# Optimization experiments

Measured on AMD Instinct MI355X. Metric: run time of the kernel, lower is better.

## Reference

```python
import jax, jax.numpy as jnp
import numpy as np

B, S, D, H, DFF = 2, 2048, 1024, 16, 4096
DK = D // H
EPS = 1e-5


def layer_norm(x, gamma, beta, eps=EPS):
    mu = jnp.mean(x, axis=-1, keepdims=True)
    var = jnp.mean(jnp.square(x - mu), axis=-1, keepdims=True)
    return (x - mu) * jax.lax.rsqrt(var + eps) * gamma + beta


def setup_inputs() -> dict:
    key = jax.random.key(0)
    ks = jax.random.split(key, 12)
    s_d = 1.0 / np.sqrt(D)
    s_f = 1.0 / np.sqrt(DFF)
    return {
        "x": jax.random.normal(ks[0], (B, S, D), jnp.float32),
        # per-head QKV projections stacked: [H, D, DK]
        "Wq": jax.random.normal(ks[1], (H, D, DK), jnp.float32) * s_d,
        "bq": jnp.zeros((H, DK), jnp.float32),
        "Wk": jax.random.normal(ks[2], (H, D, DK), jnp.float32) * s_d,
        "bk": jnp.zeros((H, DK), jnp.float32),
        "Wv": jax.random.normal(ks[3], (H, D, DK), jnp.float32) * s_d,
        "bv": jnp.zeros((H, DK), jnp.float32),
        "Wo": jax.random.normal(ks[4], (D, D), jnp.float32) * s_d,
        "bo": jnp.zeros((D,), jnp.float32),
        "W1": jax.random.normal(ks[5], (D, DFF), jnp.float32) * s_d,
        "b1": jnp.zeros((DFF,), jnp.float32),
        "W2": jax.random.normal(ks[6], (DFF, D), jnp.float32) * s_f,
        "b2": jnp.zeros((D,), jnp.float32),
        "ln1_g": jnp.ones((D,), jnp.float32),
        "ln1_b": jnp.zeros((D,), jnp.float32),
        "ln2_g": jnp.ones((D,), jnp.float32),
        "ln2_b": jnp.zeros((D,), jnp.float32),
    }


def reference(x, Wq, bq, Wk, bk, Wv, bv, Wo, bo, W1, b1, W2, b2,
              ln1_g, ln1_b, ln2_g, ln2_b):
    # --- residual 1: pre-norm multi-head self-attention (mask unused, dropout=eval) ---
    h = layer_norm(x, ln1_g, ln1_b)                      # [B,S,D]
    q = jnp.einsum('bsd,hdk->bhsk', h, Wq) + bq[:, None, :]
    k = jnp.einsum('bsd,hdk->bhsk', h, Wk) + bk[:, None, :]
    v = jnp.einsum('bsd,hdk->bhsk', h, Wv) + bv[:, None, :]
    scores = jnp.einsum('bhsk,bhtk->bhst', q, k) / np.sqrt(DK)  # [B,H,S,S]
    w = jax.nn.softmax(scores, axis=-1)
    ctx = jnp.einsum('bhst,bhtk->bhsk', w, v)            # [B,H,S,DK]
    # concat heads along feature dim -> [B,S,D]
    ctx = jnp.transpose(ctx, (0, 2, 1, 3)).reshape(B, S, D)
    attn_out = ctx @ Wo + bo
    x = x + attn_out
    # --- residual 2: pre-norm feed-forward ---
    h2 = layer_norm(x, ln2_g, ln2_b)
    ff = jax.nn.relu(h2 @ W1 + b1) @ W2 + b2
    return x + ff
```

## Files before the change

kernel.cpp:

```cpp
#include <hip/hip_runtime.h>

#define B_   2
#define S_   2048
#define D_   1024
#define H_   16
#define DK_  64
#define DFF_ 4096
#define NT_  (B_*S_)
#define QS_  3072

using u16 = unsigned short;
typedef __attribute__((ext_vector_type(8))) short bf16x8;
typedef __attribute__((ext_vector_type(4))) float f32x4;
typedef __attribute__((ext_vector_type(4))) u16  u16x4;

__device__ __forceinline__ float bf2f(u16 h) {
  union { unsigned u; float f; } c; c.u = ((unsigned)h) << 16; return c.f;
}
__device__ __forceinline__ u16 f2bf(float f) {
  union { float f; unsigned u; } c; c.f = f;
  unsigned u = c.u;
  return (u16)((u + 0x7fffu + ((u >> 16) & 1u)) >> 16);
}
__device__ __forceinline__ u16 f2bf_up(float f) {
  union { float f; unsigned u; } c; c.f = f;
  return (u16)((c.u + 0x8000u) >> 16);
}

__device__ __forceinline__ void load_lds16(const void* g, void* l) {
  __builtin_amdgcn_global_load_lds(
      (const __attribute__((address_space(1))) unsigned int*)g,
      (__attribute__((address_space(3))) unsigned int*)l, 16, 0, 0);
}

__device__ __forceinline__ void store_out(u16* p, float v)   { *p = f2bf(v); }
__device__ __forceinline__ void store_out(float* p, float v) { *p = v; }

__global__ __launch_bounds__(256) void ln_kernel(
    const float* __restrict__ x, const float* __restrict__ g,
    const float* __restrict__ bt, u16* __restrict__ o)
{
  const int row = blockIdx.x, t = threadIdx.x;
  const float4 xv = *(const float4*)(x + (size_t)row * D_ + t * 4);
  float f[4] = {xv.x, xv.y, xv.z, xv.w};
  float sum = f[0] + f[1] + f[2] + f[3];
  float sq  = f[0]*f[0] + f[1]*f[1] + f[2]*f[2] + f[3]*f[3];
#pragma unroll
  for (int d = 32; d >= 1; d >>= 1) {
    sum += __shfl_down(sum, d);
    sq  += __shfl_down(sq, d);
  }
  __shared__ float red[8];
  const int lane = t & 63, wid = t >> 6;
  if (lane == 0) { red[wid] = sum; red[wid + 4] = sq; }
  __syncthreads();
  sum = red[0] + red[1] + red[2] + red[3];
  sq  = red[4] + red[5] + red[6] + red[7];
  const float mu   = sum * (1.0f / D_);
  const float var  = sq * (1.0f / D_) - mu * mu;
  const float rstd = rsqrtf(var + 1e-5f);
  const float4 gv = *(const float4*)(g  + t * 4);
  const float4 bv = *(const float4*)(bt + t * 4);
  u16x4 ov;
  ov[0] = f2bf((f[0] - mu) * rstd * gv.x + bv.x);
  ov[1] = f2bf((f[1] - mu) * rstd * gv.y + bv.y);
  ov[2] = f2bf((f[2] - mu) * rstd * gv.z + bv.z);
  ov[3] = f2bf((f[3] - mu) * rstd * gv.w + bv.w);
  *(u16x4*)(o + (size_t)row * D_ + t * 4) = ov;
}

__global__ __launch_bounds__(256) void transpose_h(
    const float* __restrict__ in, u16* __restrict__ out, int R, int C)
{
  __shared__ float tile[32][33];
  const int z = blockIdx.z;
  const float* ip = in  + (size_t)z * R * C;
  u16*         op = out + (size_t)z * R * C;
  const int c0 = blockIdx.x * 32, r0 = blockIdx.y * 32;
  const int tx = threadIdx.x & 31, ty = threadIdx.x >> 5;
#pragma unroll
  for (int i = 0; i < 32; i += 8)
    tile[ty + i][tx] = ip[(size_t)(r0 + ty + i) * C + c0 + tx];
  __syncthreads();
#pragma unroll
  for (int i = 0; i < 32; i += 8)
    op[(size_t)(c0 + ty + i) * R + r0 + tx] = f2bf(tile[tx][ty + i]);
}

__global__ __launch_bounds__(256) void transpose_qkv(
    const float* __restrict__ Wq, const float* __restrict__ Wk,
    const float* __restrict__ Wv, u16* __restrict__ out)
{
  __shared__ float tile[32][33];
  const int z = blockIdx.z;
  const int which = z >> 4, h = z & 15;
  const float* ip = (which == 0 ? Wq : which == 1 ? Wk : Wv) + (size_t)h * 1024 * 64;
  u16* op = out + ((size_t)which * 1024 + h * 64) * 1024;
  const float sc = (which == 0) ? 0.125f : 1.0f;
  const int c0 = blockIdx.x * 32, r0 = blockIdx.y * 32;
  const int tx = threadIdx.x & 31, ty = threadIdx.x >> 5;
#pragma unroll
  for (int i = 0; i < 32; i += 8)
    tile[ty + i][tx] = ip[(size_t)(r0 + ty + i) * 64 + c0 + tx];
  __syncthreads();
#pragma unroll
  for (int i = 0; i < 32; i += 8)
    op[(size_t)(c0 + ty + i) * 1024 + r0 + tx] = f2bf(tile[tx][ty + i] * sc);
}

__global__ __launch_bounds__(256) void pack_kv(
    const u16* __restrict__ qkv, u16* __restrict__ kt, u16* __restrict__ vt)
{
  __shared__ u16 tile[32][72];
  const int z = blockIdx.y;
  const int b = z >> 4, h = z & 15;
  const int t0 = blockIdx.x * 32;
  const int tid = threadIdx.x;
  const int row = tid >> 3, sub = tid & 7;

  const u16* src = qkv + (size_t)(b * S_ + t0 + row) * QS_ + h * DK_ + sub * 8;
  *(bf16x8*)(kt + ((size_t)z * S_ + t0 + row) * 64 + sub * 8) =
      *(const bf16x8*)(src + 1024);
  *(bf16x8*)&tile[row][sub * 8] = *(const bf16x8*)(src + 2048);
  __syncthreads();

  const int d = tid >> 2, tc = (tid & 3) * 8;
  bf16x8 val;
#pragma unroll
  for (int j = 0; j < 8; ++j) val[j] = (short)tile[tc + j][d];
  *(bf16x8*)(vt + ((size_t)z * 64 + d) * S_ + t0 + tc) = val;
}

template <typename OT, int KK>
__global__ __launch_bounds__(512, 1) void gemm256(
    const u16* __restrict__ A, const u16* __restrict__ Bt,
    const float* __restrict__ bias, const float* __restrict__ biasB,
    const float* __restrict__ biasC, OT* __restrict__ C,
    int M, int N, int do_relu)
{
  constexpr int NK = KK / 32;
  __shared__ u16 lA[4][256 * 32];
  __shared__ u16 lB[4][256 * 32];
  const int tid = threadIdx.x, lane = tid & 63, wid = tid >> 6;
  const int wr = wid >> 2, wc = wid & 3;

  const int nbx = gridDim.x;
  int bid = blockIdx.y * nbx + blockIdx.x;
  const int cpx = (nbx * gridDim.y) >> 3;
  bid = (bid & 7) * cpx + (bid >> 3);
  const int row0 = (bid / nbx) * 256, col0 = (bid % nbx) * 256;

  const int c0 = tid,       sr0 = c0 >> 2, q0 = ((c0 & 3) ^ (((sr0 >> 3) & 1) << 1)) * 8;
  const int c1 = tid + 512, sr1 = c1 >> 2, q1 = ((c1 & 3) ^ (((sr1 >> 3) & 1) << 1)) * 8;
  const u16* As0 = A  + (size_t)(row0 + sr0) * KK + q0;
  const u16* As1 = A  + (size_t)(row0 + sr1) * KK + q1;
  const u16* Bs0 = Bt + (size_t)(col0 + sr0) * KK + q0;
  const u16* Bs1 = Bt + (size_t)(col0 + sr1) * KK + q1;

  f32x4 acc[8][4] = {};
  const int lrow = lane & 15, kcol = (lane >> 4) * 8;

#pragma unroll
  for (int t = 0; t < 3; ++t) {
    load_lds16(As0 + t * 32, &lA[t][c0 * 8]);
    load_lds16(Bs0 + t * 32, &lB[t][c0 * 8]);
    load_lds16(As1 + t * 32, &lA[t][c1 * 8]);
    load_lds16(Bs1 + t * 32, &lB[t][c1 * 8]);
  }
  asm volatile("s_waitcnt vmcnt(8)" ::: "memory");
  __builtin_amdgcn_sched_barrier(0);
  __builtin_amdgcn_s_barrier();

#pragma unroll 4
  for (int j = 0; j < NK; ++j) {
    const int b = j & 3;
    const u16* la = lA[b];
    const u16* lb = lB[b];
    bf16x8 af[4], bfr[4];

#pragma unroll
    for (int m = 0; m < 4; ++m) {
      const int row = wr * 128 + m * 16 + lrow;
      af[m] = *(const bf16x8*)&la[row * 32 + (kcol ^ (((row >> 3) & 1) << 4))];
    }
#pragma unroll
    for (int n = 0; n < 4; ++n) {
      const int row = wc * 64 + n * 16 + lrow;
      bfr[n] = *(const bf16x8*)&lb[row * 32 + (kcol ^ (((row >> 3) & 1) << 4))];
    }
    if (j + 3 < NK) {
      const int bb = (j + 3) & 3;
      load_lds16(As0 + (j + 3) * 32, &lA[bb][c0 * 8]);
      load_lds16(Bs0 + (j + 3) * 32, &lB[bb][c0 * 8]);
    }
    __builtin_amdgcn_s_setprio(1);
#pragma unroll
    for (int m = 0; m < 4; ++m)
#pragma unroll
      for (int n = 0; n < 4; ++n)
        acc[m][n] = __builtin_amdgcn_mfma_f32_16x16x32_bf16(af[m], bfr[n], acc[m][n], 0, 0, 0);
    __builtin_amdgcn_s_setprio(0);

#pragma unroll
    for (int m = 0; m < 4; ++m) {
      const int row = wr * 128 + (m + 4) * 16 + lrow;
      af[m] = *(const bf16x8*)&la[row * 32 + (kcol ^ (((row >> 3) & 1) << 4))];
    }
    if (j + 3 < NK) {
      const int bb = (j + 3) & 3;
      load_lds16(As1 + (j + 3) * 32, &lA[bb][c1 * 8]);
      load_lds16(Bs1 + (j + 3) * 32, &lB[bb][c1 * 8]);
    }
    __builtin_amdgcn_s_setprio(1);
#pragma unroll
    for (int m = 0; m < 4; ++m)
#pragma unroll
      for (int n = 0; n < 4; ++n)
        acc[m + 4][n] = __builtin_amdgcn_mfma_f32_16x16x32_bf16(af[m], bfr[n], acc[m + 4][n], 0, 0, 0);
    __builtin_amdgcn_s_setprio(0);
    if (j + 3 < NK)      { asm volatile("s_waitcnt vmcnt(8)" ::: "memory"); }
    else if (j + 2 < NK) { asm volatile("s_waitcnt vmcnt(4)" ::: "memory"); }
    else if (j + 1 < NK) { asm volatile("s_waitcnt vmcnt(0)" ::: "memory"); }
    __builtin_amdgcn_sched_barrier(0);
    __builtin_amdgcn_s_barrier();
  }

#pragma unroll
  for (int m = 0; m < 8; ++m)
#pragma unroll
    for (int n = 0; n < 4; ++n) {
      const int rbase = row0 + wr*128 + m*16 + ((lane >> 4) << 2);
      const int c     = col0 + wc*64 + n*16 + (lane & 15);
      float bv = 0.f;
      if (biasC)      bv = c < 1024 ? bias[c] * 0.125f
                         : (c < 2048 ? biasB[c - 1024] : biasC[c - 2048]);
      else if (bias)  bv = bias[c];
#pragma unroll
      for (int r = 0; r < 4; ++r) {
        float vv = acc[m][n][r] + bv;
        if (do_relu) vv = vv > 0.f ? vv : 0.f;
        store_out(&C[(size_t)(rbase + r) * N + c], vv);
      }
    }
}

template <int KK>
__global__ __launch_bounds__(512, 1) void gemm256pk(
    const u16* __restrict__ A, const u16* __restrict__ Bt,
    u16* __restrict__ P, int M, int N, int Ktot)
{
  constexpr int NK = KK / 32;
  __shared__ u16 lA[4][256 * 32];
  __shared__ u16 lB[4][256 * 32];
  const int tid = threadIdx.x, lane = tid & 63, wid = tid >> 6;
  const int wr = wid >> 2, wc = wid & 3;

  const int nbx = gridDim.x;
  int bid = blockIdx.y * nbx + blockIdx.x;
  const int cpx = (nbx * gridDim.y) >> 3;
  bid = (bid & 7) * cpx + (bid >> 3);
  const int row0 = (bid / nbx) * 256, col0 = (bid % nbx) * 256;
  const int kb = blockIdx.z * KK;

  const int c0 = tid,       sr0 = c0 >> 2, q0 = ((c0 & 3) ^ (((sr0 >> 3) & 1) << 1)) * 8;
  const int c1 = tid + 512, sr1 = c1 >> 2, q1 = ((c1 & 3) ^ (((sr1 >> 3) & 1) << 1)) * 8;
  const u16* As0 = A  + (size_t)(row0 + sr0) * Ktot + kb + q0;
  const u16* As1 = A  + (size_t)(row0 + sr1) * Ktot + kb + q1;
  const u16* Bs0 = Bt + (size_t)(col0 + sr0) * Ktot + kb + q0;
  const u16* Bs1 = Bt + (size_t)(col0 + sr1) * Ktot + kb + q1;

  f32x4 acc[8][4] = {};
  const int lrow = lane & 15, kcol = (lane >> 4) * 8;

#pragma unroll
  for (int t = 0; t < 3; ++t) {
    load_lds16(As0 + t * 32, &lA[t][c0 * 8]);
    load_lds16(Bs0 + t * 32, &lB[t][c0 * 8]);
    load_lds16(As1 + t * 32, &lA[t][c1 * 8]);
    load_lds16(Bs1 + t * 32, &lB[t][c1 * 8]);
  }
  asm volatile("s_waitcnt vmcnt(8)" ::: "memory");
  __builtin_amdgcn_sched_barrier(0);
  __builtin_amdgcn_s_barrier();

#pragma unroll 4
  for (int j = 0; j < NK; ++j) {
    const int b = j & 3;
    const u16* la = lA[b];
    const u16* lb = lB[b];
    bf16x8 af[4], bfr[4];

#pragma unroll
    for (int m = 0; m < 4; ++m) {
      const int row = wr * 128 + m * 16 + lrow;
      af[m] = *(const bf16x8*)&la[row * 32 + (kcol ^ (((row >> 3) & 1) << 4))];
    }
#pragma unroll
    for (int n = 0; n < 4; ++n) {
      const int row = wc * 64 + n * 16 + lrow;
      bfr[n] = *(const bf16x8*)&lb[row * 32 + (kcol ^ (((row >> 3) & 1) << 4))];
    }
    if (j + 3 < NK) {
      const int bb = (j + 3) & 3;
      load_lds16(As0 + (j + 3) * 32, &lA[bb][c0 * 8]);
      load_lds16(Bs0 + (j + 3) * 32, &lB[bb][c0 * 8]);
    }
    __builtin_amdgcn_s_setprio(1);
#pragma unroll
    for (int m = 0; m < 4; ++m)
#pragma unroll
      for (int n = 0; n < 4; ++n)
        acc[m][n] = __builtin_amdgcn_mfma_f32_16x16x32_bf16(af[m], bfr[n], acc[m][n], 0, 0, 0);
    __builtin_amdgcn_s_setprio(0);

#pragma unroll
    for (int m = 0; m < 4; ++m) {
      const int row = wr * 128 + (m + 4) * 16 + lrow;
      af[m] = *(const bf16x8*)&la[row * 32 + (kcol ^ (((row >> 3) & 1) << 4))];
    }
    if (j + 3 < NK) {
      const int bb = (j + 3) & 3;
      load_lds16(As1 + (j + 3) * 32, &lA[bb][c1 * 8]);
      load_lds16(Bs1 + (j + 3) * 32, &lB[bb][c1 * 8]);
    }
    __builtin_amdgcn_s_setprio(1);
#pragma unroll
    for (int m = 0; m < 4; ++m)
#pragma unroll
      for (int n = 0; n < 4; ++n)
        acc[m + 4][n] = __builtin_amdgcn_mfma_f32_16x16x32_bf16(af[m], bfr[n], acc[m + 4][n], 0, 0, 0);
    __builtin_amdgcn_s_setprio(0);
    if (j + 3 < NK)      { asm volatile("s_waitcnt vmcnt(8)" ::: "memory"); }
    else if (j + 2 < NK) { asm volatile("s_waitcnt vmcnt(4)" ::: "memory"); }
    else if (j + 1 < NK) { asm volatile("s_waitcnt vmcnt(0)" ::: "memory"); }
    __builtin_amdgcn_sched_barrier(0);
    __builtin_amdgcn_s_barrier();
  }

  u16* Pz = P + (size_t)blockIdx.z * M * N;
#pragma unroll
  for (int m = 0; m < 8; ++m)
#pragma unroll
    for (int n = 0; n < 4; ++n) {
      const int rbase = row0 + wr*128 + m*16 + ((lane >> 4) << 2);
      const int c     = col0 + wc*64 + n*16 + (lane & 15);
#pragma unroll
      for (int r = 0; r < 4; ++r)
        Pz[(size_t)(rbase + r) * N + c] = f2bf(acc[m][n][r]);
    }
}

template <typename OT>
__global__ __launch_bounds__(256) void gemm_bt64(
    const u16* __restrict__ A, const u16* __restrict__ Bt,
    const float* __restrict__ bias, const float* __restrict__ res,
    OT* __restrict__ C, int M, int N, int K, int do_relu)
{
  __shared__ u16 lA[2][128 * 32];
  __shared__ u16 lB[2][64 * 32];
  const int tid = threadIdx.x, lane = tid & 63, wid = tid >> 6;

  const int nbx = gridDim.x;
  int bid = blockIdx.y * nbx + blockIdx.x;
  const int cpx = (nbx * gridDim.y) >> 3;
  bid = (bid & 7) * cpx + (bid >> 3);
  const int row0 = (bid / nbx) * 128, col0 = (bid % nbx) * 64;

  f32x4 acc[2][4] = {};

  const int cc0 = tid, cc1 = tid + 256;
  const int r0 = cc0 >> 2, s0 = cc0 & 3;
  const int r1 = cc1 >> 2, s1 = cc1 & 3;
  const int ko0 = (s0 ^ ((r0 >> 1) & 3)) * 8;
  const int ko1 = (s1 ^ ((r1 >> 1) & 3)) * 8;

#define GST64(bf, k0)                                                         \
  {                                                                           \
    load_lds16(A  + (size_t)(row0 + r0) * K + (k0) + ko0, &lA[bf][cc0 * 8]);  \
    load_lds16(A  + (size_t)(row0 + r1) * K + (k0) + ko1, &lA[bf][cc1 * 8]);  \
    load_lds16(Bt + (size_t)(col0 + r0) * K + (k0) + ko0, &lB[bf][cc0 * 8]);  \
  }

  const int nk = K >> 5;
  GST64(0, 0);
  int cur = 0;
  for (int t = 0; t < nk; ++t) {
    __syncthreads();
    if (t + 1 < nk) GST64(cur ^ 1, (t + 1) * 32);
    bf16x8 af[2], bfr[4];
#pragma unroll
    for (int m = 0; m < 2; ++m) {
      const int row = wid * 32 + m * 16 + (lane & 15);
      af[m] = *(const bf16x8*)&lA[cur][row * 32 + (((lane >> 4) ^ ((row >> 1) & 3)) * 8)];
    }
#pragma unroll
    for (int n = 0; n < 4; ++n) {
      const int row = n * 16 + (lane & 15);
      bfr[n] = *(const bf16x8*)&lB[cur][row * 32 + (((lane >> 4) ^ ((row >> 1) & 3)) * 8)];
    }
#pragma unroll
    for (int m = 0; m < 2; ++m)
#pragma unroll
      for (int n = 0; n < 4; ++n)
        acc[m][n] = __builtin_amdgcn_mfma_f32_16x16x32_bf16(af[m], bfr[n], acc[m][n], 0, 0, 0);
    cur ^= 1;
  }
#undef GST64

#pragma unroll
  for (int m = 0; m < 2; ++m)
#pragma unroll
    for (int n = 0; n < 4; ++n) {
      const int rbase = row0 + wid*32 + m*16 + ((lane >> 4) << 2);
      const int c     = col0 + n*16 + (lane & 15);
      const float bv  = bias ? bias[c] : 0.f;
#pragma unroll
      for (int r = 0; r < 4; ++r) {
        const int rr = rbase + r;
        float vv = acc[m][n][r] + bv;
        if (res) vv += res[(size_t)rr * N + c];
        if (do_relu) vv = vv > 0.f ? vv : 0.f;
        store_out(&C[(size_t)rr * N + c], vv);
      }
    }
}

__global__ __launch_bounds__(256) void ffr_reduce4(
    const u16* __restrict__ P, const float* __restrict__ x1,
    const float* __restrict__ b2, float* __restrict__ out)
{
  const size_t i = (size_t)blockIdx.x * 256 + threadIdx.x;
  const size_t M4 = (size_t)NT_ * D_;
  const float4 r  = ((const float4*)x1)[i];
  const float4 bb = ((const float4*)b2)[i & 255];
  float o0 = r.x + bb.x, o1 = r.y + bb.y, o2 = r.z + bb.z, o3 = r.w + bb.w;
#pragma unroll
  for (int z = 0; z < 4; ++z) {
    const u16x4 p = *(const u16x4*)(P + z * M4 + i * 4);
    o0 += bf2f(p[0]); o1 += bf2f(p[1]); o2 += bf2f(p[2]); o3 += bf2f(p[3]);
  }
  float4 o; o.x = o0; o.y = o1; o.z = o2; o.w = o3;
  ((float4*)out)[i] = o;
}

__global__ __launch_bounds__(512) void attn_kernel(
    const u16* __restrict__ QKV, const u16* __restrict__ Kt,
    const u16* __restrict__ Vt, u16* __restrict__ O)
{
  __shared__ u16 lK[2][64 * 64];
  __shared__ u16 lV[2][64 * 64];
  __shared__ u16 lP[128 * 64];

  const int tid = threadIdx.x, lane = tid & 63, wid = tid >> 6;
  const int g  = (blockIdx.x & 7) * 64 + (blockIdx.x >> 3);
  const int qt = g & 15, h = (g >> 4) & 15, b = g >> 8;
  const int z  = b * H_ + h;

  const u16* Qp  = QKV + (size_t)(b * S_ + qt * 128) * QS_ + h * DK_;
  const u16* Kpb = Kt + (size_t)z * S_ * 64;
  const u16* Vb  = Vt + (size_t)z * DK_ * S_;

  bf16x8 qf[2];
  {
    const int qr = wid * 16 + (lane & 15);
    qf[0] = *(const bf16x8*)(Qp + (size_t)qr * QS_ + (lane >> 4) * 8);
    qf[1] = *(const bf16x8*)(Qp + (size_t)qr * QS_ + 32 + (lane >> 4) * 8);
  }

  const bf16x8 vone = {16256,16256,16256,16256,16256,16256,16256,16256};

#define STAGE_KV(bf, kt_)                                                     \
  {                                                                           \
    const u16* Kp = Kpb + (size_t)(kt_) * 64 * 64;                            \
    const u16* Vp = Vb + (size_t)(kt_) * 64;                                  \
    const int c = tid, r = c >> 3, sub = c & 7;                               \
    load_lds16(Kp + r * 64 + ((sub ^ (r & 7)) * 8), &lK[bf][c * 8]);          \
    load_lds16(Vp + (size_t)r * S_ + ((sub ^ (r & 7)) * 8), &lV[bf][c * 8]);  \
  }

  float m_run = -1e30f;
  f32x4 l_acc = {};
  f32x4 o_acc[4] = {};

  STAGE_KV(0, 0);
  int cur = 0;

  for (int kt = 0; kt < S_ / 64; ++kt) {
    __syncthreads();
    if (kt + 1 < S_ / 64) STAGE_KV(cur ^ 1, kt + 1);

    f32x4 s[4];
    __builtin_amdgcn_s_setprio(1);
#pragma unroll
    for (int kf = 0; kf < 4; ++kf) {
      const int row = kf * 16 + (lane & 15);
      const int i0 = (row * 64 + (lane >> 4) * 8)      ^ ((row & 7) << 3);
      const int i1 = (row * 64 + 32 + (lane >> 4) * 8) ^ ((row & 7) << 3);
      bf16x8 k0 = *(const bf16x8*)&lK[cur][i0];
      bf16x8 k1 = *(const bf16x8*)&lK[cur][i1];
      f32x4 sc = {};
      sc = __builtin_amdgcn_mfma_f32_16x16x32_bf16(k0, qf[0], sc, 0, 0, 0);
      sc = __builtin_amdgcn_mfma_f32_16x16x32_bf16(k1, qf[1], sc, 0, 0, 0);
      s[kf] = sc;
    }
    __builtin_amdgcn_s_setprio(0);

    float t0 = fmaxf(fmaxf(s[0][0], s[0][1]), fmaxf(s[0][2], s[0][3]));
    float t1 = fmaxf(fmaxf(s[1][0], s[1][1]), fmaxf(s[1][2], s[1][3]));
    float t2 = fmaxf(fmaxf(s[2][0], s[2][1]), fmaxf(s[2][2], s[2][3]));
    float t3 = fmaxf(fmaxf(s[3][0], s[3][1]), fmaxf(s[3][2], s[3][3]));
    float pmax = fmaxf(fmaxf(t0, t1), fmaxf(t2, t3));
    pmax = fmaxf(pmax, __shfl_xor(pmax, 16));
    pmax = fmaxf(pmax, __shfl_xor(pmax, 32));

    const bool grow = pmax > m_run + 8.0f;
    const float mnew = grow ? pmax : m_run;
    if (__any(grow)) {
      const float scale = __expf(m_run - mnew);
#pragma unroll
      for (int r = 0; r < 4; ++r) {
        const float sr = __shfl(scale, (lane >> 4) * 4 + r);
        l_acc[r] *= sr;
#pragma unroll
        for (int nf = 0; nf < 4; ++nf) o_acc[nf][r] *= sr;
      }
    }
    m_run = mnew;

    const int prow = wid * 16 + (lane & 15);
#pragma unroll
    for (int kf = 0; kf < 4; ++kf) {
      u16x4 pk;
#pragma unroll
      for (int r = 0; r < 4; ++r) pk[r] = f2bf_up(__expf(s[kf][r] - m_run));
      const int idx = (prow * 64 + kf * 16 + (lane >> 4) * 4) ^ ((prow & 7) << 3);
      *(u16x4*)&lP[idx] = pk;
    }
    asm volatile("s_waitcnt lgkmcnt(0)" ::: "memory");
    __builtin_amdgcn_sched_barrier(0);

    bf16x8 pa0 = *(const bf16x8*)&lP[(prow * 64 + (lane >> 4) * 8)      ^ ((prow & 7) << 3)];
    bf16x8 pa1 = *(const bf16x8*)&lP[(prow * 64 + 32 + (lane >> 4) * 8) ^ ((prow & 7) << 3)];
    __builtin_amdgcn_s_setprio(1);
    l_acc = __builtin_amdgcn_mfma_f32_16x16x32_bf16(pa0, vone, l_acc, 0, 0, 0);
    l_acc = __builtin_amdgcn_mfma_f32_16x16x32_bf16(pa1, vone, l_acc, 0, 0, 0);
#pragma unroll
    for (int nf = 0; nf < 4; ++nf) {
      const int vrow = nf * 16 + (lane & 15);
      bf16x8 v0 = *(const bf16x8*)&lV[cur][(vrow * 64 + (lane >> 4) * 8)      ^ ((vrow & 7) << 3)];
      bf16x8 v1 = *(const bf16x8*)&lV[cur][(vrow * 64 + 32 + (lane >> 4) * 8) ^ ((vrow & 7) << 3)];
      o_acc[nf] = __builtin_amdgcn_mfma_f32_16x16x32_bf16(pa0, v0, o_acc[nf], 0, 0, 0);
      o_acc[nf] = __builtin_amdgcn_mfma_f32_16x16x32_bf16(pa1, v1, o_acc[nf], 0, 0, 0);
    }
    __builtin_amdgcn_s_setprio(0);
    cur ^= 1;
  }

#pragma unroll
  for (int nf = 0; nf < 4; ++nf)
#pragma unroll
    for (int r = 0; r < 4; ++r) {
      const int qrow = qt * 128 + wid * 16 + (lane >> 4) * 4 + r;
      const int col  = h * DK_ + nf * 16 + (lane & 15);
      O[(size_t)(b * S_ + qrow) * D_ + col] = f2bf(o_acc[nf][r] / l_acc[r]);
    }
}

extern "C" void kernel_launch(void* const* d_in, const int* in_sizes, int n_in,
                              void* d_out, int out_size, void* d_ws, size_t ws_size,
                              hipStream_t stream)
{
  const float* x   = (const float*)d_in[0];
  const float* Wq  = (const float*)d_in[1];
  const float* bq  = (const float*)d_in[2];
  const float* Wk  = (const float*)d_in[3];
  const float* bk  = (const float*)d_in[4];
  const float* Wv  = (const float*)d_in[5];
  const float* bv  = (const float*)d_in[6];
  const float* Wo  = (const float*)d_in[7];
  const float* bo  = (const float*)d_in[8];
  const float* W1  = (const float*)d_in[9];
  const float* b1  = (const float*)d_in[10];
  const float* W2  = (const float*)d_in[11];
  const float* b2  = (const float*)d_in[12];
  const float* g1  = (const float*)d_in[13];
  const float* be1 = (const float*)d_in[14];
  const float* g2  = (const float*)d_in[15];
  const float* be2 = (const float*)d_in[16];
  float* out = (float*)d_out;

  const size_t MB = 1024 * 1024;
  char* base = (char*)d_ws;
  u16*   xn    = (u16*)(base);
  u16*   qkv   = (u16*)(base +  8*MB);
  u16*   ctx   = (u16*)(base + 32*MB);
  float* x1    = (float*)(base + 40*MB);
  u16*   vt    = (u16*)(base + 40*MB);
  u16*   kt    = (u16*)(base + 48*MB);
  u16*   ff1   = (u16*)(base +  8*MB);
  u16*   wqkvT = (u16*)(base + 56*MB);
  u16*   woT   = (u16*)(base + 62*MB);
  u16*   w1T   = (u16*)(base + 64*MB);
  u16*   w2T   = (u16*)(base + 72*MB);
  u16*   pkh   = (u16*)(base + 80*MB);

  const bool splitk = ws_size >= (size_t)112 * MB;

  dim3 blk(256);
  transpose_qkv<<<dim3(2, 32, 48), blk, 0, stream>>>(Wq, Wk, Wv, wqkvT);
  transpose_h<<<dim3(32, 32, 1),  blk, 0, stream>>>(Wo, woT, 1024, 1024);
  transpose_h<<<dim3(128, 32, 1), blk, 0, stream>>>(W1, w1T, 1024, 4096);
  transpose_h<<<dim3(32, 128, 1), blk, 0, stream>>>(W2, w2T, 4096, 1024);

  ln_kernel<<<NT_, blk, 0, stream>>>(x, g1, be1, xn);

  gemm256<u16, 1024><<<dim3(12, 16), dim3(512), 0, stream>>>(
      xn, wqkvT, bq, bk, bv, qkv, NT_, QS_, 0);

  pack_kv<<<dim3(S_ / 32, B_ * H_), blk, 0, stream>>>(qkv, kt, vt);

  attn_kernel<<<dim3(512), dim3(512), 0, stream>>>(qkv, kt, vt, ctx);

  gemm_bt64<<<dim3(16, 32), blk, 0, stream>>>(ctx, woT, bo, x, x1, NT_, D_, D_, 0);

  ln_kernel<<<NT_, blk, 0, stream>>>(x1, g2, be2, xn);

  gemm256<u16, 1024><<<dim3(16, 16), dim3(512), 0, stream>>>(
      xn, w1T, b1, (const float*)nullptr, (const float*)nullptr, ff1, NT_, DFF_, 1);

  if (splitk) {
    gemm256pk<1024><<<dim3(4, 16, 4), dim3(512), 0, stream>>>(
        ff1, w2T, pkh, NT_, D_, DFF_);
    ffr_reduce4<<<dim3(4096), blk, 0, stream>>>(pkh, x1, b2, out);
  } else {
    gemm_bt64<<<dim3(16, 32), blk, 0, stream>>>(ff1, w2T, b2, x1, out, NT_, D_, DFF_, 0);
  }
}
```

Before: 258.3 us.

## Widen attention KV tile to 128 and restructure K/V staging schedule

The flash-attention kernel now processes 128 keys per iteration instead of 64, halving loop iterations, barriers and online-softmax rescale checks. K is single-buffered and restaged after a mid-iteration barrier, while V stays double-buffered, to fit the larger tiles in LDS. A launch-bounds occupancy hint is added. In exchange each iteration holds more score registers, adds a second __syncthreads per iteration, and raises LDS use.

```diff
diff --git a/kernel.cpp b/kernel.cpp
--- a/kernel.cpp
+++ b/kernel.cpp
@@ -443,13 +443,13 @@
   ((float4*)out)[i] = o;
 }
 
-__global__ __launch_bounds__(512) void attn_kernel(
+__global__ __launch_bounds__(512, 4) void attn_kernel(
     const u16* __restrict__ QKV, const u16* __restrict__ Kt,
     const u16* __restrict__ Vt, u16* __restrict__ O)
 {
-  __shared__ u16 lK[2][64 * 64];
-  __shared__ u16 lV[2][64 * 64];
-  __shared__ u16 lP[128 * 64];
+  __shared__ u16 lK[128 * 64];
+  __shared__ u16 lV[2][64 * 128];
+  __shared__ u16 lP[128 * 128];
 
   const int tid = threadIdx.x, lane = tid & 63, wid = tid >> 6;
   const int g  = (blockIdx.x & 7) * 64 + (blockIdx.x >> 3);
@@ -460,44 +460,55 @@
   const u16* Kpb = Kt + (size_t)z * S_ * 64;
   const u16* Vb  = Vt + (size_t)z * DK_ * S_;
 
+  const int hi = lane >> 4;
+
   bf16x8 qf[2];
   {
     const int qr = wid * 16 + (lane & 15);
-    qf[0] = *(const bf16x8*)(Qp + (size_t)qr * QS_ + (lane >> 4) * 8);
-    qf[1] = *(const bf16x8*)(Qp + (size_t)qr * QS_ + 32 + (lane >> 4) * 8);
+    qf[0] = *(const bf16x8*)(Qp + (size_t)qr * QS_ + hi * 8);
+    qf[1] = *(const bf16x8*)(Qp + (size_t)qr * QS_ + 32 + hi * 8);
   }
 
   const bf16x8 vone = {16256,16256,16256,16256,16256,16256,16256,16256};
 
-#define STAGE_KV(bf, kt_)                                                     \
+#define STAGE_K(kt_)                                                          \
   {                                                                           \
-    const u16* Kp = Kpb + (size_t)(kt_) * 64 * 64;                            \
-    const u16* Vp = Vb + (size_t)(kt_) * 64;                                  \
-    const int c = tid, r = c >> 3, sub = c & 7;                               \
-    load_lds16(Kp + r * 64 + ((sub ^ (r & 7)) * 8), &lK[bf][c * 8]);          \
-    load_lds16(Vp + (size_t)r * S_ + ((sub ^ (r & 7)) * 8), &lV[bf][c * 8]);  \
+    const u16* Kp = Kpb + (size_t)(kt_) * 128 * 64;                           \
+    _Pragma("unroll")                                                         \
+    for (int i = 0; i < 2; ++i) {                                             \
+      const int c = tid + i * 512, r = c >> 3, sub = c & 7;                   \
+      load_lds16(Kp + r * 64 + ((sub ^ (r & 7)) * 8), &lK[c * 8]);            \
+    }                                                                         \
+  }
+#define STAGE_V(bf, kt_)                                                      \
+  {                                                                           \
+    const u16* Vp = Vb + (size_t)(kt_) * 128;                                 \
+    _Pragma("unroll")                                                         \
+    for (int i = 0; i < 2; ++i) {                                             \
+      const int c = tid + i * 512, r = c >> 4, sub = c & 15;                  \
+      load_lds16(Vp + (size_t)r * S_ + ((sub ^ (r & 7)) * 8), &lV[bf][c * 8]); \
+    }                                                                         \
   }
 
   float m_run = -1e30f;
   f32x4 l_acc = {};
   f32x4 o_acc[4] = {};
 
-  STAGE_KV(0, 0);
-  int cur = 0;
-
-  for (int kt = 0; kt < S_ / 64; ++kt) {
+  STAGE_K(0);
+  STAGE_V(0, 0);
+  int vcur = 0;
+
+  for (int kt = 0; kt < S_ / 128; ++kt) {
     __syncthreads();
-    if (kt + 1 < S_ / 64) STAGE_KV(cur ^ 1, kt + 1);
-
-    f32x4 s[4];
+    if (kt + 1 < S_ / 128) STAGE_V(vcur ^ 1, kt + 1);
+
+    f32x4 s[8];
     __builtin_amdgcn_s_setprio(1);
 #pragma unroll
-    for (int kf = 0; kf < 4; ++kf) {
+    for (int kf = 0; kf < 8; ++kf) {
       const int row = kf * 16 + (lane & 15);
-      const int i0 = (row * 64 + (lane >> 4) * 8)      ^ ((row & 7) << 3);
-      const int i1 = (row * 64 + 32 + (lane >> 4) * 8) ^ ((row & 7) << 3);
-      bf16x8 k0 = *(const bf16x8*)&lK[cur][i0];
-      bf16x8 k1 = *(const bf16x8*)&lK[cur][i1];
+      bf16x8 k0 = *(const bf16x8*)&lK[(row * 64 + hi * 8)      ^ ((row & 7) << 3)];
+      bf16x8 k1 = *(const bf16x8*)&lK[(row * 64 + 32 + hi * 8) ^ ((row & 7) << 3)];
       f32x4 sc = {};
       sc = __builtin_amdgcn_mfma_f32_16x16x32_bf16(k0, qf[0], sc, 0, 0, 0);
       sc = __builtin_amdgcn_mfma_f32_16x16x32_bf16(k1, qf[1], sc, 0, 0, 0);
@@ -505,11 +516,12 @@
     }
     __builtin_amdgcn_s_setprio(0);
 
-    float t0 = fmaxf(fmaxf(s[0][0], s[0][1]), fmaxf(s[0][2], s[0][3]));
-    float t1 = fmaxf(fmaxf(s[1][0], s[1][1]), fmaxf(s[1][2], s[1][3]));
-    float t2 = fmaxf(fmaxf(s[2][0], s[2][1]), fmaxf(s[2][2], s[2][3]));
-    float t3 = fmaxf(fmaxf(s[3][0], s[3][1]), fmaxf(s[3][2], s[3][3]));
-    float pmax = fmaxf(fmaxf(t0, t1), fmaxf(t2, t3));
+    float pmax = -1e30f;
+#pragma unroll
+    for (int kf = 0; kf < 8; ++kf) {
+      const float t = fmaxf(fmaxf(s[kf][0], s[kf][1]), fmaxf(s[kf][2], s[kf][3]));
+      pmax = fmaxf(pmax, t);
+    }
     pmax = fmaxf(pmax, __shfl_xor(pmax, 16));
     pmax = fmaxf(pmax, __shfl_xor(pmax, 32));
 
@@ -519,7 +531,7 @@
       const float scale = __expf(m_run - mnew);
 #pragma unroll
       for (int r = 0; r < 4; ++r) {
-        const float sr = __shfl(scale, (lane >> 4) * 4 + r);
+        const float sr = __shfl(scale, hi * 4 + r);
         l_acc[r] *= sr;
 #pragma unroll
         for (int nf = 0; nf < 4; ++nf) o_acc[nf][r] *= sr;
@@ -529,38 +541,44 @@
 
     const int prow = wid * 16 + (lane & 15);
 #pragma unroll
-    for (int kf = 0; kf < 4; ++kf) {
+    for (int kf = 0; kf < 8; ++kf) {
       u16x4 pk;
 #pragma unroll
       for (int r = 0; r < 4; ++r) pk[r] = f2bf_up(__expf(s[kf][r] - m_run));
-      const int idx = (prow * 64 + kf * 16 + (lane >> 4) * 4) ^ ((prow & 7) << 3);
+      const int idx = (prow * 128 + kf * 16 + hi * 4) ^ ((prow & 7) << 3);
       *(u16x4*)&lP[idx] = pk;
     }
-    asm volatile("s_waitcnt lgkmcnt(0)" ::: "memory");
-    __builtin_amdgcn_sched_barrier(0);
-
-    bf16x8 pa0 = *(const bf16x8*)&lP[(prow * 64 + (lane >> 4) * 8)      ^ ((prow & 7) << 3)];
-    bf16x8 pa1 = *(const bf16x8*)&lP[(prow * 64 + 32 + (lane >> 4) * 8) ^ ((prow & 7) << 3)];
+
+    __syncthreads();
+    if (kt + 1 < S_ / 128) STAGE_K(kt + 1);
+
+    bf16x8 pa[4];
+#pragma unroll
+    for (int si = 0; si < 4; ++si)
+      pa[si] = *(const bf16x8*)&lP[(prow * 128 + si * 32 + hi * 8) ^ ((prow & 7) << 3)];
+
     __builtin_amdgcn_s_setprio(1);
-    l_acc = __builtin_amdgcn_mfma_f32_16x16x32_bf16(pa0, vone, l_acc, 0, 0, 0);
-    l_acc = __builtin_amdgcn_mfma_f32_16x16x32_bf16(pa1, vone, l_acc, 0, 0, 0);
+#pragma unroll
+    for (int si = 0; si < 4; ++si)
+      l_acc = __builtin_amdgcn_mfma_f32_16x16x32_bf16(pa[si], vone, l_acc, 0, 0, 0);
 #pragma unroll
     for (int nf = 0; nf < 4; ++nf) {
       const int vrow = nf * 16 + (lane & 15);
-      bf16x8 v0 = *(const bf16x8*)&lV[cur][(vrow * 64 + (lane >> 4) * 8)      ^ ((vrow & 7) << 3)];
-      bf16x8 v1 = *(const bf16x8*)&lV[cur][(vrow * 64 + 32 + (lane >> 4) * 8) ^ ((vrow & 7) << 3)];
-      o_acc[nf] = __builtin_amdgcn_mfma_f32_16x16x32_bf16(pa0, v0, o_acc[nf], 0, 0, 0);
-      o_acc[nf] = __builtin_amdgcn_mfma_f32_16x16x32_bf16(pa1, v1, o_acc[nf], 0, 0, 0);
+#pragma unroll
+      for (int si = 0; si < 4; ++si) {
+        bf16x8 v = *(const bf16x8*)&lV[vcur][(vrow * 128 + si * 32 + hi * 8) ^ ((vrow & 7) << 3)];
+        o_acc[nf] = __builtin_amdgcn_mfma_f32_16x16x32_bf16(pa[si], v, o_acc[nf], 0, 0, 0);
+      }
     }
     __builtin_amdgcn_s_setprio(0);
-    cur ^= 1;
+    vcur ^= 1;
   }
 
 #pragma unroll
   for (int nf = 0; nf < 4; ++nf)
 #pragma unroll
     for (int r = 0; r < 4; ++r) {
-      const int qrow = qt * 128 + wid * 16 + (lane >> 4) * 4 + r;
+      const int qrow = qt * 128 + wid * 16 + hi * 4 + r;
       const int col  = h * DK_ + nf * 16 + (lane & 15);
       O[(size_t)(b * S_ + qrow) * D_ + col] = f2bf(o_acc[nf][r] / l_acc[r]);
     }
```

New measurement: 259.5 us. About the same (+0.4%).
